# Kernel optimization log

Hardware: AMD Instinct MI355X
Metric: run time of the kernel (lower is better)

## Reference

```python
import jax, jax.numpy as jnp
import numpy as np

N_NODES = 50000
N_EDGES = 800000
LN_EPS = 1e-5


def _segment_softmax_aggr(msg, t, dst, n):
    # SoftmaxAggregation(learn=True): alpha = softmax(msg * t) per dest segment, out = sum(alpha * msg)
    logits = msg * t  # [E, C]
    m = jax.ops.segment_max(logits, dst, num_segments=n)
    m = jnp.where(jnp.isfinite(m), m, 0.0)  # empty segments -> 0 to keep exp finite
    e = jnp.exp(logits - m[dst])
    denom = jax.ops.segment_sum(e, dst, num_segments=n)
    alpha = e / jnp.maximum(denom[dst], 1e-16)
    return jax.ops.segment_sum(alpha * msg, dst, num_segments=n)


def _sage_conv(x, src, dst, wp, bp, t, wl, bl, wr):
    # project=True: messages come from relu(lin(x)); root term uses ORIGINAL x
    xp = jax.nn.relu(x @ wp + bp)
    msg = xp[src]                                   # [E, C] gather
    aggr = _segment_softmax_aggr(msg, t, dst, x.shape[0])
    out = aggr @ wl + bl + x @ wr
    # normalize=True: L2 normalize rows (eps as in F.normalize)
    nrm = jnp.maximum(jnp.linalg.norm(out, axis=-1, keepdims=True), 1e-12)
    return out / nrm


def _mem_pool(x, k, w_conv, wl, bl):
    # PyG MemPooling, tau=1: Student-t kernel 1/(1+d^2)
    H, K, F = k.shape
    kk = k.reshape(H * K, F)
    d2 = (jnp.sum(kk * kk, -1)[:, None] + jnp.sum(x * x, -1)[None, :]
          - 2.0 * kk @ x.T)                          # [H*K, N]
    d2 = jnp.maximum(d2, 0.0)
    dist = 1.0 / (1.0 + d2)
    dist = dist.reshape(H, K, -1).transpose(0, 2, 1)  # [H, N, K]
    S = dist / jnp.sum(dist, -1, keepdims=True)       # per-head normalize over clusters
    S = jnp.einsum('h,hnk->nk', w_conv, S)            # 1x1 conv mixing heads (no bias)
    S = jax.nn.softmax(S, axis=-1)                    # [N, K]
    xp = S.T @ x                                      # [K, F]
    return xp @ wl + bl                               # [K, out]


def setup_inputs() -> dict:
    key = jax.random.key(0)
    ks = jax.random.split(key, 20)
    rn = lambda i, shp, s: jax.random.normal(ks[i], shp, dtype=jnp.float32) * s
    inp = {
        'x': rn(0, (N_NODES, 64), 1.0),
        'edge_index': jax.random.randint(ks[1], (2, N_EDGES), 0, N_NODES, dtype=jnp.int32),
        'w_proj1': rn(2, (64, 64), 0.1), 'b_proj1': rn(3, (64,), 0.05),
        't1': jnp.ones((64,), jnp.float32),
        'w_l1': rn(4, (64, 256), 0.1), 'b_l1': rn(5, (256,), 0.05),
        'w_r1': rn(6, (64, 256), 0.1),
        'w_proj2': rn(7, (256, 256), 0.05), 'b_proj2': rn(8, (256,), 0.05),
        't2': jnp.ones((256,), jnp.float32),
        'w_l2': rn(9, (256, 128), 0.05), 'b_l2': rn(10, (128,), 0.05),
        'w_r2': rn(11, (256, 128), 0.05),
        'k_mem': rn(12, (4, 4, 128), 1.0),
        'w_conv': rn(13, (4,), 0.5),
        'w_memlin': rn(14, (128, 128), 0.08), 'b_memlin': rn(15, (128,), 0.05),
        'w_fx': rn(16, (128, 64), 0.08), 'b_fx': rn(17, (64,), 0.05),
        'gamma': jnp.ones((64,), jnp.float32),
        'beta': jnp.zeros((64,), jnp.float32),
    }
    return inp


def reference(x, edge_index, w_proj1, b_proj1, t1, w_l1, b_l1, w_r1,
              w_proj2, b_proj2, t2, w_l2, b_l2, w_r2,
              k_mem, w_conv, w_memlin, b_memlin, w_fx, b_fx, gamma, beta):
    src, dst = edge_index[0], edge_index[1]
    h = _sage_conv(x, src, dst, w_proj1, b_proj1, t1, w_l1, b_l1, w_r1)
    h = jax.nn.relu(h)                              # dropout = identity (eval)
    h = _sage_conv(h, src, dst, w_proj2, b_proj2, t2, w_l2, b_l2, w_r2)
    h = jax.nn.relu(h)
    pooled = _mem_pool(h, k_mem, w_conv, w_memlin, b_memlin)  # [4, 128]
    g = jnp.mean(pooled, axis=0, keepdims=True)     # global_mean_pool -> [1, 128]
    y = g @ w_fx + b_fx                             # [1, 64]
    mu = jnp.mean(y, -1, keepdims=True)
    var = jnp.var(y, -1, keepdims=True)
    y = (y - mu) / jnp.sqrt(var + LN_EPS) * gamma + beta
    return jax.nn.relu(y)
```

## Files before the change

### kernel.cpp

```cpp
#include <hip/hip_runtime.h>
#include <hip/hip_bf16.h>

#define N_NODES 50000
#define N_EDGES 800000
#define NB 196
#define PC_SLICES 2048
#define NWAVES 8192

typedef __attribute__((ext_vector_type(8))) short short8;
typedef __attribute__((ext_vector_type(4))) float f32x4;
typedef __attribute__((ext_vector_type(2))) float f32x2;

#define QSCALE2 (2.f / 255.f)
#define QINV2   127.5f
#define QSCALE1 (12.75f / 255.f)
#define QINV1   20.f

__device__ __forceinline__ float us2f(unsigned short u) {
    return __uint_as_float(((unsigned int)u) << 16);
}
__device__ __forceinline__ unsigned short f2bu(float f) {
    unsigned int u = __float_as_uint(f);
    unsigned int r = (u + 0x7fffu + ((u >> 16) & 1u)) >> 16;
    return (unsigned short)r;
}
__device__ __forceinline__ float exp2_hw(float x) {
    float r;
    __asm__("v_exp_f32 %0, %1" : "=v"(r) : "v"(x));
    return r;
}
__device__ __forceinline__ void async16(const void* g, void* l) {
    __builtin_amdgcn_global_load_lds(
        (const __attribute__((address_space(1))) unsigned int*)g,
        (__attribute__((address_space(3))) unsigned int*)l, 16, 0, 0);
}
#define LOG2E 1.44269504088896f

__global__ void k_hist(const int* __restrict__ dst, int* __restrict__ counts) {
    int e = blockIdx.x * 256 + threadIdx.x;
    if (e < N_EDGES) atomicAdd(&counts[dst[e]], 1);
}

__global__ __launch_bounds__(256) void k_scan1(const int* __restrict__ counts,
                                               int* __restrict__ row_ptr,
                                               int* __restrict__ partial) {
    __shared__ int sd[256];
    int t = threadIdx.x, i = blockIdx.x * 256 + t;
    int v = (i < N_NODES) ? counts[i] : 0;
    sd[t] = v;
    __syncthreads();
    for (int off = 1; off < 256; off <<= 1) {
        int o = (t >= off) ? sd[t - off] : 0;
        __syncthreads();
        sd[t] += o;
        __syncthreads();
    }
    if (i < N_NODES) row_ptr[i] = sd[t] - v;
    if (t == 255) partial[blockIdx.x] = sd[255];
}

__global__ __launch_bounds__(256) void k_scan3b(int* __restrict__ row_ptr,
                                                const int* __restrict__ partial,
                                                int* __restrict__ cursor) {
    __shared__ int sd[256];
    int t = threadIdx.x;
    sd[t] = (t < blockIdx.x) ? partial[t] : 0;
    __syncthreads();
    for (int off = 128; off > 0; off >>= 1) {
        if (t < off) sd[t] += sd[t + off];
        __syncthreads();
    }
    int base = sd[0];
    int i = blockIdx.x * 256 + t;
    if (i < N_NODES) {
        int v = row_ptr[i] + base;
        row_ptr[i] = v;
        cursor[i] = v;
    }
    if (blockIdx.x == 0 && t == 0) row_ptr[N_NODES] = N_EDGES;
}

__global__ void k_scatter(const int* __restrict__ src, const int* __restrict__ dst,
                          int* __restrict__ cursor, int* __restrict__ src_sorted) {
    int e = blockIdx.x * 256 + threadIdx.x;
    if (e < N_EDGES) {
        int d = dst[e];
        int pos = atomicAdd(&cursor[d], 1);
        src_sorted[pos] = src[e];
    }
}

__global__ __launch_bounds__(256) void k_split(const int* __restrict__ row_ptr,
                                               int* __restrict__ split) {
    int w = blockIdx.x * 256 + threadIdx.x;
    if (w > NWAVES) return;
    if (w == NWAVES) { split[w] = N_NODES; return; }
    int target = (int)((long long)w * N_EDGES / NWAVES);
    int lo = 0, hi = N_NODES;
    while (lo < hi) {
        int mid = (lo + hi) >> 1;
        if (row_ptr[mid] < target) lo = mid + 1; else hi = mid;
    }
    split[w] = lo;
}

#define XCAST_N (N_NODES * 64)
#define PREP_TOT (XCAST_N + 167936)
__global__ __launch_bounds__(256) void k_prep(const float* __restrict__ x,
                                              const float* __restrict__ wp1,
                                              const float* __restrict__ wl1,
                                              const float* __restrict__ wr1,
                                              const float* __restrict__ wp2,
                                              const float* __restrict__ wl2,
                                              const float* __restrict__ wr2,
                                              unsigned short* __restrict__ cat1,
                                              unsigned short* __restrict__ B0T,
                                              unsigned short* __restrict__ B1T,
                                              unsigned short* __restrict__ BP2T,
                                              unsigned short* __restrict__ B2T) {
    int idx = (blockIdx.x * 256 + threadIdx.x) * 4;
    if (idx < XCAST_N) {
        int i = idx >> 6, j = idx & 63;
        float4 v = *(const float4*)&x[idx];
        ushort4 o = { f2bu(v.x), f2bu(v.y), f2bu(v.z), f2bu(v.w) };
        *(ushort4*)&cat1[i * 128 + 64 + j] = o;
        return;
    }
    int w = idx - XCAST_N;
    if (w < 4096)  { float4 v = *(const float4*)&wp1[w]; int k = w >> 6, n = w & 63;
                     B0T[n*64+k]=f2bu(v.x); B0T[(n+1)*64+k]=f2bu(v.y);
                     B0T[(n+2)*64+k]=f2bu(v.z); B0T[(n+3)*64+k]=f2bu(v.w); return; }
    w -= 4096;
    if (w < 16384) { float4 v = *(const float4*)&wl1[w]; int k = w >> 8, n = w & 255;
                     B1T[n*128+k]=f2bu(v.x); B1T[(n+1)*128+k]=f2bu(v.y);
                     B1T[(n+2)*128+k]=f2bu(v.z); B1T[(n+3)*128+k]=f2bu(v.w); return; }
    w -= 16384;
    if (w < 16384) { float4 v = *(const float4*)&wr1[w]; int k = w >> 8, n = w & 255;
                     B1T[n*128+64+k]=f2bu(v.x); B1T[(n+1)*128+64+k]=f2bu(v.y);
                     B1T[(n+2)*128+64+k]=f2bu(v.z); B1T[(n+3)*128+64+k]=f2bu(v.w); return; }
    w -= 16384;
    if (w < 65536) { float4 v = *(const float4*)&wp2[w]; int k = w >> 8, n = w & 255;
                     BP2T[n*256+k]=f2bu(v.x); BP2T[(n+1)*256+k]=f2bu(v.y);
                     BP2T[(n+2)*256+k]=f2bu(v.z); BP2T[(n+3)*256+k]=f2bu(v.w); return; }
    w -= 65536;
    if (w < 32768) { float4 v = *(const float4*)&wl2[w]; int k = w >> 7, n = w & 127;
                     B2T[n*512+k]=f2bu(v.x); B2T[(n+1)*512+k]=f2bu(v.y);
                     B2T[(n+2)*512+k]=f2bu(v.z); B2T[(n+3)*512+k]=f2bu(v.w); return; }
    w -= 32768;
    if (w < 32768) { float4 v = *(const float4*)&wr2[w]; int k = w >> 7, n = w & 127;
                     B2T[n*512+256+k]=f2bu(v.x); B2T[(n+1)*512+256+k]=f2bu(v.y);
                     B2T[(n+2)*512+256+k]=f2bu(v.z); B2T[(n+3)*512+256+k]=f2bu(v.w); return; }
}

template<int K, int C, int LDA, int LDOUT, int OUT_OFF, int EP, int WPB, int MH>
__global__ __launch_bounds__(256, WPB) void k_gemm(const unsigned short* __restrict__ A,
                                                   const unsigned short* __restrict__ BT,
                                                   const float* __restrict__ bias,
                                                   void* __restrict__ outv,
                                                   const float* __restrict__ kmem,
                                                   const float* __restrict__ wconv,
                                                   float* __restrict__ Sm,
                                                   float qinv) {
    constexpr int NT = C / 16;
    constexpr int SAE = 64 * MH * 64;
    constexpr int SBE = C * 64;
    constexpr int STAGE_B = (SAE + SBE) * 2;
    constexpr int RPLD = (EP == 2) ? (C + 4) : ((EP == 3) ? (C + 16) : (C + 8));
    constexpr int RP_B = 64 * RPLD * (EP == 2 ? 4 : (EP == 3 ? 1 : 2));
    constexpr int SMEM_B = STAGE_B > RP_B ? STAGE_B : RP_B;
    constexpr int POOL_B = (EP == 2) ? (2048 * 4 + 64 + 16) : 16;
    __shared__ __align__(16) char smem[SMEM_B + POOL_B];
    unsigned short* sA = (unsigned short*)smem;
    unsigned short* sB = sA + SAE;
    float* kls  = (float*)(smem + SMEM_B);
    float* kk2s = kls + 2048;
    float* wcs  = kk2s + 16;

    int t = threadIdx.x;
    int wid = t >> 6, lane = t & 63;
    int lrow = lane & 15, quad = lane >> 4;
    int m0 = blockIdx.x * (64 * MH);

    if (EP == 2) {
        for (int i = t; i < 2048; i += 256) kls[i] = kmem[i];
        if (t < 4) wcs[t] = wconv[t];
        __syncthreads();
        if (t < 16) {
            float s = 0.f;
            for (int f = 0; f < 128; ++f) { float v = kls[t * 128 + f]; s += v * v; }
            kk2s[t] = s;
        }
    }

    f32x4 acc[MH][NT];
#pragma unroll
    for (int h = 0; h < MH; ++h)
#pragma unroll
        for (int nt = 0; nt < NT; ++nt)
#pragma unroll
            for (int r = 0; r < 4; ++r) acc[h][nt][r] = 0.f;

    for (int k0 = 0; k0 < K; k0 += 64) {
        __syncthreads();
        for (int i = t; i < 64 * MH * 8; i += 256) {
            int r = i >> 3, seg = i & 7;
            size_t m = (size_t)(m0 + r);
            async16(&A[m * LDA + k0 + ((seg ^ (r & 7)) << 3)],
                    (char*)sA + (size_t)(i - lane) * 16);
        }
        for (int i = t; i < C * 8; i += 256) {
            int n = i >> 3, seg = i & 7;
            async16(&BT[(size_t)n * K + k0 + ((seg ^ (n & 7)) << 3)],
                    (char*)sB + (size_t)(i - lane) * 16);
        }
        __syncthreads();
#pragma unroll
        for (int kk = 0; kk < 2; ++kk) {
            int sw = lrow & 7;
            short8 av[MH];
#pragma unroll
            for (int h = 0; h < MH; ++h)
                av[h] = *(const short8*)&sA[(h * 64 + wid * 16 + lrow) * 64 +
                                            (((kk * 4 + quad) ^ sw) << 3)];
#pragma unroll
            for (int nt = 0; nt < NT; ++nt) {
                short8 bfg = *(const short8*)&sB[(nt * 16 + lrow) * 64 +
                                                 (((kk * 4 + quad) ^ sw) << 3)];
#pragma unroll
                for (int h = 0; h < MH; ++h)
                    acc[h][nt] = __builtin_amdgcn_mfma_f32_16x16x32_bf16(av[h], bfg, acc[h][nt], 0, 0, 0);
            }
        }
    }

#pragma unroll
    for (int h = 0; h < MH; ++h) {
#pragma unroll
        for (int nt = 0; nt < NT; ++nt) {
            float bv = bias[nt * 16 + lrow];
#pragma unroll
            for (int r = 0; r < 4; ++r) acc[h][nt][r] += bv;
        }
        if (EP == 1 || EP == 2) {
#pragma unroll
            for (int r = 0; r < 4; ++r) {
                float ss = 0.f;
#pragma unroll
                for (int nt = 0; nt < NT; ++nt) ss += acc[h][nt][r] * acc[h][nt][r];
                ss += __shfl_xor(ss, 1);
                ss += __shfl_xor(ss, 2);
                ss += __shfl_xor(ss, 4);
                ss += __shfl_xor(ss, 8);
                float rinv = 1.f / fmaxf(sqrtf(ss), 1e-12f);
#pragma unroll
                for (int nt = 0; nt < NT; ++nt)
                    acc[h][nt][r] = fmaxf(acc[h][nt][r] * rinv, 0.f);
            }
        } else {
#pragma unroll
            for (int nt = 0; nt < NT; ++nt)
#pragma unroll
                for (int r = 0; r < 4; ++r) acc[h][nt][r] = fmaxf(acc[h][nt][r], 0.f);
        }
    }

    __syncthreads();
#pragma unroll
    for (int h = 0; h < MH; ++h) {
        if (EP == 2) {
            float* rp = (float*)smem;
#pragma unroll
            for (int nt = 0; nt < NT; ++nt)
#pragma unroll
                for (int r = 0; r < 4; ++r)
                    rp[(wid * 16 + quad * 4 + r) * RPLD + nt * 16 + lrow] = acc[h][nt][r];
            __syncthreads();
            float* outp = (float*)outv;
            for (int i = t; i < 64 * C / 4; i += 256) {
                int f = i * 4, r = f / C, c = f % C;
                int m = m0 + h * 64 + r;
                if (m < N_NODES)
                    *(float4*)&outp[(size_t)m * LDOUT + OUT_OFF + c] = *(const float4*)&rp[r * RPLD + c];
            }
            {
                int row = t >> 2, p = t & 3;
                int cbase = p * 32;
                float dots[16];
#pragma unroll
                for (int k = 0; k < 16; ++k) dots[k] = 0.f;
                float x2 = 0.f;
#pragma unroll
                for (int j = 0; j < 8; ++j) {
                    int c4 = (j + p * 2) & 7;
                    float4 xv = *(const float4*)&rp[row * RPLD + cbase + c4 * 4];
                    x2 += xv.x * xv.x + xv.y * xv.y + xv.z * xv.z + xv.w * xv.w;
#pragma unroll
                    for (int k = 0; k < 16; ++k) {
                        float4 kv = *(const float4*)&kls[k * 128 + cbase + c4 * 4];
                        dots[k] += xv.x * kv.x + xv.y * kv.y + xv.z * kv.z + xv.w * kv.w;
                    }
                }
#pragma unroll
                for (int k = 0; k < 16; ++k) {
                    dots[k] += __shfl_xor(dots[k], 1);
                    dots[k] += __shfl_xor(dots[k], 2);
                }
                x2 += __shfl_xor(x2, 1);
                x2 += __shfl_xor(x2, 2);
                if (p == 0) {
                    int m = m0 + h * 64 + row;
                    if (m < N_NODES) {
                        float dist[16];
#pragma unroll
                        for (int k = 0; k < 16; ++k) {
                            float d2 = fmaxf(kk2s[k] + x2 - 2.f * dots[k], 0.f);
                            dist[k] = 1.f / (1.f + d2);
                        }
                        float s0 = 0.f, s1 = 0.f, s2 = 0.f, s3 = 0.f;
#pragma unroll
                        for (int hh = 0; hh < 4; ++hh) {
                            float den = dist[hh * 4] + dist[hh * 4 + 1] +
                                        dist[hh * 4 + 2] + dist[hh * 4 + 3];
                            float inv = wcs[hh] / den;
                            s0 += dist[hh * 4 + 0] * inv;
                            s1 += dist[hh * 4 + 1] * inv;
                            s2 += dist[hh * 4 + 2] * inv;
                            s3 += dist[hh * 4 + 3] * inv;
                        }
                        float mx = fmaxf(fmaxf(s0, s1), fmaxf(s2, s3));
                        float e0 = __expf(s0 - mx), e1 = __expf(s1 - mx);
                        float e2 = __expf(s2 - mx), e3 = __expf(s3 - mx);
                        float inv = 1.f / (e0 + e1 + e2 + e3);
                        *(float4*)&Sm[(size_t)m * 4] =
                            make_float4(e0 * inv, e1 * inv, e2 * inv, e3 * inv);
                    }
                }
            }
            __syncthreads();
        } else if (EP == 3) {
            unsigned char* rp = (unsigned char*)smem;
#pragma unroll
            for (int nt = 0; nt < NT; ++nt)
#pragma unroll
                for (int r = 0; r < 4; ++r) {
                    float q = fminf(__builtin_rintf(acc[h][nt][r] * qinv), 255.f);
                    rp[(wid * 16 + quad * 4 + r) * RPLD + nt * 16 + lrow] = (unsigned char)(int)q;
                }
            __syncthreads();
            unsigned char* outp = (unsigned char*)outv;
            for (int i = t; i < 64 * C / 16; i += 256) {
                int f = i * 16, r = f / C, c = f % C;
                int m = m0 + h * 64 + r;
                if (m < N_NODES)
                    *(uint4*)&outp[(size_t)m * LDOUT + OUT_OFF + c] = *(const uint4*)&rp[r * RPLD + c];
            }
            __syncthreads();
        } else {
            unsigned short* rp = (unsigned short*)smem;
#pragma unroll
            for (int nt = 0; nt < NT; ++nt)
#pragma unroll
                for (int r = 0; r < 4; ++r)
                    rp[(wid * 16 + quad * 4 + r) * RPLD + nt * 16 + lrow] = f2bu(acc[h][nt][r]);
            __syncthreads();
            unsigned short* outp = (unsigned short*)outv;
            for (int i = t; i < 64 * C / 8; i += 256) {
                int f = i * 8, r = f / C, c = f % C;
                int m = m0 + h * 64 + r;
                if (m < N_NODES)
                    *(uint4*)&outp[(size_t)m * LDOUT + OUT_OFF + c] = *(const uint4*)&rp[r * RPLD + c];
            }
            __syncthreads();
        }
    }
}

__global__ __launch_bounds__(256, 4) void k_aggr256(const unsigned char* __restrict__ xp,
                                                    const float* __restrict__ tvec,
                                                    const int* __restrict__ row_ptr,
                                                    const int* __restrict__ srcs,
                                                    const int* __restrict__ split,
                                                    unsigned short* __restrict__ outp) {
    int t = threadIdx.x & 63;
    int w = blockIdx.x * 4 + (threadIdx.x >> 6);
    float4 tv4 = *(const float4*)&tvec[t * 4];
    f32x2 tv01 = {tv4.x * (LOG2E * QSCALE2), tv4.y * (LOG2E * QSCALE2)};
    f32x2 tv23 = {tv4.z * (LOG2E * QSCALE2), tv4.w * (LOG2E * QSCALE2)};
    int n    = __builtin_amdgcn_readfirstlane(split[w]);
    int nend = __builtin_amdgcn_readfirstlane(split[w + 1]);
    if (n >= nend) return;
    int e    = __builtin_amdgcn_readfirstlane(row_ptr[n]);
    int eend = __builtin_amdgcn_readfirstlane(row_ptr[nend]);
    int rp_next = __builtin_amdgcn_readfirstlane(row_ptr[n + 1]);
    f32x2 se01 = {0.f, 0.f}, se23 = {0.f, 0.f};
    f32x2 sem01 = {0.f, 0.f}, sem23 = {0.f, 0.f};

#define FINALIZE()                                                             \
    {                                                                          \
        ushort4 o;                                                             \
        o.x = f2bu(QSCALE2 * sem01.x / fmaxf(se01.x, 1e-16f));                 \
        o.y = f2bu(QSCALE2 * sem01.y / fmaxf(se01.y, 1e-16f));                 \
        o.z = f2bu(QSCALE2 * sem23.x / fmaxf(se23.x, 1e-16f));                 \
        o.w = f2bu(QSCALE2 * sem23.y / fmaxf(se23.y, 1e-16f));                 \
        *(ushort4*)&outp[(size_t)n * 512 + t * 4] = o;                         \
        se01 = (f32x2){0.f, 0.f}; se23 = (f32x2){0.f, 0.f};                    \
        sem01 = (f32x2){0.f, 0.f}; sem23 = (f32x2){0.f, 0.f};                  \
        ++n;                                                                   \
        rp_next = (n < nend) ? __builtin_amdgcn_readfirstlane(row_ptr[n + 1])  \
                             : 0x7FFFFFFF;                                     \
    }
#define EDGE_BODY(VV)                                                          \
    {                                                                          \
        f32x2 m01 = {(float)((VV) & 0xFFu), (float)(((VV) >> 8) & 0xFFu)};     \
        f32x2 m23 = {(float)(((VV) >> 16) & 0xFFu), (float)((VV) >> 24)};      \
        f32x2 l01 = m01 * tv01, l23 = m23 * tv23;                              \
        f32x2 w01, w23;                                                        \
        w01.x = exp2_hw(l01.x); w01.y = exp2_hw(l01.y);                        \
        w23.x = exp2_hw(l23.x); w23.y = exp2_hw(l23.y);                        \
        se01 += w01; se23 += w23;                                              \
        sem01 = __builtin_elementwise_fma(w01, m01, sem01);                    \
        sem23 = __builtin_elementwise_fma(w23, m23, sem23);                    \
    }

    while (rp_next <= e) FINALIZE();

    while (e < eend) {
        unsigned int v[16];
        int rem = eend - e;
        int cnt = rem > 16 ? 16 : rem;
        if (cnt == 16) {
#pragma unroll
            for (int j = 0; j < 16; ++j) {
                const unsigned char* p = xp + (size_t)srcs[e + j] * 256;
                v[j] = *(const unsigned int*)&p[t * 4];
            }
        } else {
#pragma unroll
            for (int j = 0; j < 16; ++j) {
                int ee = e + j;
                ee = ee < eend ? ee : eend - 1;
                const unsigned char* p = xp + (size_t)srcs[ee] * 256;
                v[j] = *(const unsigned int*)&p[t * 4];
            }
        }
#pragma unroll
        for (int j = 0; j < 16; ++j) {
            if (j < cnt) {
                EDGE_BODY(v[j])
                while (e + j + 1 == rp_next) FINALIZE();
            }
        }
        e += cnt;
    }
#undef EDGE_BODY
#undef FINALIZE
}

__global__ __launch_bounds__(256, 4) void k_aggr64(const unsigned char* __restrict__ xp,
                                                   const float* __restrict__ tvec,
                                                   const int* __restrict__ row_ptr,
                                                   const int* __restrict__ srcs,
                                                   const int* __restrict__ split,
                                                   unsigned short* __restrict__ outp) {
    int c = threadIdx.x & 63;
    int w = blockIdx.x * 4 + (threadIdx.x >> 6);
    float tv = tvec[c] * (LOG2E * QSCALE1);
    int n    = __builtin_amdgcn_readfirstlane(split[w]);
    int nend = __builtin_amdgcn_readfirstlane(split[w + 1]);
    if (n >= nend) return;
    int e    = __builtin_amdgcn_readfirstlane(row_ptr[n]);
    int eend = __builtin_amdgcn_readfirstlane(row_ptr[nend]);
    int rp_next = __builtin_amdgcn_readfirstlane(row_ptr[n + 1]);
    float se = 0.f, sem = 0.f;

#define FIN1()                                                                 \
    {                                                                          \
        outp[(size_t)n * 128 + c] = f2bu(QSCALE1 * sem / fmaxf(se, 1e-16f));   \
        se = 0.f; sem = 0.f;                                                   \
        ++n;                                                                   \
        rp_next = (n < nend) ? __builtin_amdgcn_readfirstlane(row_ptr[n + 1])  \
                             : 0x7FFFFFFF;                                     \
    }

    while (rp_next <= e) FIN1();

    while (e < eend) {
        unsigned char v[16];
        int rem = eend - e;
        int cnt = rem > 16 ? 16 : rem;
        if (cnt == 16) {
#pragma unroll
            for (int j = 0; j < 16; ++j)
                v[j] = xp[(size_t)srcs[e + j] * 64 + c];
        } else {
#pragma unroll
            for (int j = 0; j < 16; ++j) {
                int ee = e + j;
                ee = ee < eend ? ee : eend - 1;
                v[j] = xp[(size_t)srcs[ee] * 64 + c];
            }
        }
#pragma unroll
        for (int j = 0; j < 16; ++j) {
            if (j < cnt) {
                float msg = (float)v[j];
                float wv = exp2_hw(msg * tv);
                se += wv;
                sem = fmaf(wv, msg, sem);
                while (e + j + 1 == rp_next) FIN1();
            }
        }
        e += cnt;
    }
#undef FIN1
}

__global__ __launch_bounds__(256) void k_pool_c(const float* __restrict__ h2,
                                                const float* __restrict__ Sm,
                                                float* __restrict__ part) {
    int t = threadIdx.x;
    int c = t & 127, sub = t >> 7;
    int slice = blockIdx.x * 2 + sub;
    float a0 = 0.f, a1 = 0.f, a2 = 0.f, a3 = 0.f;
    for (int n = slice; n < N_NODES; n += PC_SLICES) {
        float xv = h2[(size_t)n * 128 + c];
        float4 sv = *(const float4*)&Sm[(size_t)n * 4];
        a0 = fmaf(sv.x, xv, a0);
        a1 = fmaf(sv.y, xv, a1);
        a2 = fmaf(sv.z, xv, a2);
        a3 = fmaf(sv.w, xv, a3);
    }
    float* p = &part[(size_t)slice * 512];
    p[0 * 128 + c] = a0;
    p[1 * 128 + c] = a1;
    p[2 * 128 + c] = a2;
    p[3 * 128 + c] = a3;
}

__global__ __launch_bounds__(256) void k_pool_b(const float* __restrict__ part,
                                                float* __restrict__ pooled) {
    int j = blockIdx.x;
    float s = 0.f;
    for (int b = threadIdx.x; b < PC_SLICES; b += 256) s += part[(size_t)b * 512 + j];
#pragma unroll
    for (int off = 32; off > 0; off >>= 1) s += __shfl_xor(s, off);
    __shared__ float red[4];
    int lane = threadIdx.x & 63, wid = threadIdx.x >> 6;
    if (lane == 0) red[wid] = s;
    __syncthreads();
    if (threadIdx.x == 0) pooled[j] = red[0] + red[1] + red[2] + red[3];
}

__global__ __launch_bounds__(128) void k_final(const float* __restrict__ pooled,
                                               const float* __restrict__ wmem,
                                               const float* __restrict__ bmem,
                                               const float* __restrict__ wfx,
                                               const float* __restrict__ bfx,
                                               const float* __restrict__ gamma,
                                               const float* __restrict__ beta,
                                               float* __restrict__ out) {
    __shared__ float gx[128], g[128];
    int t = threadIdx.x;
    gx[t] = 0.25f * (pooled[t] + pooled[128 + t] + pooled[256 + t] + pooled[384 + t]);
    __syncthreads();
    float acc = bmem[t];
    for (int f = 0; f < 128; ++f) acc = fmaf(gx[f], wmem[f * 128 + t], acc);
    g[t] = acc;
    __syncthreads();
    if (t < 64) {
        float y = bfx[t];
        for (int f = 0; f < 128; ++f) y = fmaf(g[f], wfx[f * 64 + t], y);
        float s = y, s2 = y * y;
#pragma unroll
        for (int off = 32; off > 0; off >>= 1) {
            s += __shfl_xor(s, off);
            s2 += __shfl_xor(s2, off);
        }
        float mu = s * (1.f / 64.f);
        float var = s2 * (1.f / 64.f) - mu * mu;
        float v = (y - mu) / sqrtf(var + 1e-5f) * gamma[t] + beta[t];
        out[t] = fmaxf(v, 0.f);
    }
}

extern "C" void kernel_launch(void* const* d_in, const int* in_sizes, int n_in,
                              void* d_out, int out_size, void* d_ws, size_t ws_size,
                              hipStream_t stream) {
    const float* x        = (const float*)d_in[0];
    const int*   ei       = (const int*)  d_in[1];
    const float* w_proj1  = (const float*)d_in[2];
    const float* b_proj1  = (const float*)d_in[3];
    const float* t1       = (const float*)d_in[4];
    const float* w_l1     = (const float*)d_in[5];
    const float* b_l1     = (const float*)d_in[6];
    const float* w_r1     = (const float*)d_in[7];
    const float* w_proj2  = (const float*)d_in[8];
    const float* b_proj2  = (const float*)d_in[9];
    const float* t2       = (const float*)d_in[10];
    const float* w_l2     = (const float*)d_in[11];
    const float* b_l2     = (const float*)d_in[12];
    const float* w_r2     = (const float*)d_in[13];
    const float* k_mem    = (const float*)d_in[14];
    const float* w_conv   = (const float*)d_in[15];
    const float* w_memlin = (const float*)d_in[16];
    const float* b_memlin = (const float*)d_in[17];
    const float* w_fx     = (const float*)d_in[18];
    const float* b_fx     = (const float*)d_in[19];
    const float* gamma    = (const float*)d_in[20];
    const float* beta     = (const float*)d_in[21];
    const int* src = ei;
    const int* dst = ei + N_EDGES;
    (void)in_sizes; (void)n_in; (void)out_size; (void)ws_size;

    char* W = (char*)d_ws;
    const size_t MB = 1024 * 1024;
    int*   row_ptr    = (int*)(W + 0);
    int*   cursor     = (int*)(W + 256 * 1024);
    int*   partial    = (int*)(W + 512 * 1024);
    int*   split      = (int*)(W + 520 * 1024);
    int*   src_sorted = (int*)(W + 768 * 1024);
    unsigned short* cat1 = (unsigned short*)(W + 4 * MB);
    unsigned char*  xp1  = (unsigned char*)(W + 17 * MB);
    unsigned short* cat2 = (unsigned short*)(W + 24 * MB);
    unsigned char*  xp2  = (unsigned char*)(W + 76 * MB);
    float* h2     = (float*)(W + 102 * MB);
    float* Sm     = (float*)(W + 128 * MB);
    float* pooled = (float*)(W + 131 * MB);
    unsigned short* B0T  = (unsigned short*)(W + 133 * MB);
    unsigned short* B1T  = (unsigned short*)(W + 134 * MB);
    unsigned short* BP2T = (unsigned short*)(W + 135 * MB);
    unsigned short* B2T  = (unsigned short*)(W + 136 * MB);
    float* part   = (float*)(W + 140 * MB);

    hipMemsetAsync(cursor, 0, N_NODES * sizeof(int), stream);
    k_hist<<<(N_EDGES + 255) / 256, 256, 0, stream>>>(dst, cursor);
    k_scan1<<<NB, 256, 0, stream>>>(cursor, row_ptr, partial);
    k_scan3b<<<NB, 256, 0, stream>>>(row_ptr, partial, cursor);
    k_split<<<(NWAVES + 1 + 255) / 256, 256, 0, stream>>>(row_ptr, split);
    k_scatter<<<(N_EDGES + 255) / 256, 256, 0, stream>>>(src, dst, cursor, src_sorted);

    k_prep<<<(PREP_TOT / 4 + 255) / 256, 256, 0, stream>>>(
        x, w_proj1, w_l1, w_r1, w_proj2, w_l2, w_r2, cat1, B0T, B1T, BP2T, B2T);

    const int GB = (N_NODES + 127) / 128;
    const int AGB = NWAVES / 4;

    k_gemm<64, 64, 128, 64, 0, 3, 4, 2><<<GB, 256, 0, stream>>>(
        cat1 + 64, B0T, b_proj1, xp1, nullptr, nullptr, nullptr, QINV1);
    k_aggr64<<<AGB, 256, 0, stream>>>(xp1, t1, row_ptr, src_sorted, split, cat1);
    k_gemm<128, 256, 128, 512, 256, 1, 3, 2><<<GB, 256, 0, stream>>>(
        cat1, B1T, b_l1, cat2, nullptr, nullptr, nullptr, 0.f);

    k_gemm<256, 256, 512, 256, 0, 3, 3, 2><<<GB, 256, 0, stream>>>(
        cat2 + 256, BP2T, b_proj2, xp2, nullptr, nullptr, nullptr, QINV2);
    k_aggr256<<<AGB, 256, 0, stream>>>(xp2, t2, row_ptr, src_sorted, split, cat2);
    k_gemm<512, 128, 512, 128, 0, 2, 3, 2><<<GB, 256, 0, stream>>>(
        cat2, B2T, b_l2, h2, k_mem, w_conv, Sm, 0.f);

    k_pool_c<<<PC_SLICES / 2, 256, 0, stream>>>(h2, Sm, part);
    k_pool_b<<<512, 256, 0, stream>>>(part, pooled);
    k_final<<<1, 128, 0, stream>>>(pooled, w_memlin, b_memlin, w_fx, b_fx, gamma, beta,
                                   (float*)d_out);
}
```

Baseline: 376.7 us.

## Replace global per-node atomic scatter with two-level bucketed CSR build

The CSR construction now works in two passes. Edges are first bucketed by destination block of 256 nodes using 196 global atomic counters, with src and the local dst offset packed into one int. A per-block kernel then scatters inside each bucket using shared-memory atomics. The aim is to replace scattered global atomics and random writes with more local access, at the cost of an extra pass, an extra launch and a temporary buffer. Packing src into 16 bits assumes node ids stay below 65536.

```diff
diff --git a/kernel.cpp b/kernel.cpp
--- a/kernel.cpp
+++ b/kernel.cpp
@@ -60,8 +60,7 @@
 }
 
 __global__ __launch_bounds__(256) void k_scan3b(int* __restrict__ row_ptr,
-                                                const int* __restrict__ partial,
-                                                int* __restrict__ cursor) {
+                                                const int* __restrict__ partial) {
     __shared__ int sd[256];
     int t = threadIdx.x;
     sd[t] = (t < blockIdx.x) ? partial[t] : 0;
@@ -72,21 +71,39 @@
     }
     int base = sd[0];
     int i = blockIdx.x * 256 + t;
-    if (i < N_NODES) {
-        int v = row_ptr[i] + base;
-        row_ptr[i] = v;
-        cursor[i] = v;
-    }
+    if (i < N_NODES) row_ptr[i] += base;
     if (blockIdx.x == 0 && t == 0) row_ptr[N_NODES] = N_EDGES;
 }
 
-__global__ void k_scatter(const int* __restrict__ src, const int* __restrict__ dst,
-                          int* __restrict__ cursor, int* __restrict__ src_sorted) {
+__global__ void k_binit(const int* __restrict__ row_ptr, int* __restrict__ bcur) {
+    int b = threadIdx.x;
+    if (b < NB) bcur[b] = row_ptr[b * 256];
+}
+
+__global__ void k_bucket(const int* __restrict__ src, const int* __restrict__ dst,
+                         int* __restrict__ bcur, int* __restrict__ tmp) {
     int e = blockIdx.x * 256 + threadIdx.x;
     if (e < N_EDGES) {
         int d = dst[e];
-        int pos = atomicAdd(&cursor[d], 1);
-        src_sorted[pos] = src[e];
+        int pos = atomicAdd(&bcur[d >> 8], 1);
+        tmp[pos] = src[e] | ((d & 255) << 16);
+    }
+}
+
+__global__ __launch_bounds__(256) void k_scatter2(const int* __restrict__ row_ptr,
+                                                  const int* __restrict__ tmp,
+                                                  int* __restrict__ src_sorted) {
+    __shared__ int lcur[256];
+    int b = blockIdx.x, t = threadIdx.x;
+    int n0 = b * 256;
+    int nhi = n0 + 256 < N_NODES ? n0 + 256 : N_NODES;
+    if (n0 + t < nhi) lcur[t] = row_ptr[n0 + t];
+    __syncthreads();
+    int ebeg = row_ptr[n0], eend = row_ptr[nhi];
+    for (int i = ebeg + t; i < eend; i += 256) {
+        int w = tmp[i];
+        int pos = atomicAdd(&lcur[(w >> 16) & 255], 1);
+        src_sorted[pos] = w & 0xFFFF;
     }
 }
 
@@ -615,8 +632,9 @@
     char* W = (char*)d_ws;
     const size_t MB = 1024 * 1024;
     int*   row_ptr    = (int*)(W + 0);
-    int*   cursor     = (int*)(W + 256 * 1024);
+    int*   counts     = (int*)(W + 256 * 1024);
     int*   partial    = (int*)(W + 512 * 1024);
+    int*   bcur       = (int*)(W + 512 * 1024 + 4096);
     int*   split      = (int*)(W + 520 * 1024);
     int*   src_sorted = (int*)(W + 768 * 1024);
     unsigned short* cat1 = (unsigned short*)(W + 4 * MB);
@@ -631,13 +649,16 @@
     unsigned short* BP2T = (unsigned short*)(W + 135 * MB);
     unsigned short* B2T  = (unsigned short*)(W + 136 * MB);
     float* part   = (float*)(W + 140 * MB);
-
-    hipMemsetAsync(cursor, 0, N_NODES * sizeof(int), stream);
-    k_hist<<<(N_EDGES + 255) / 256, 256, 0, stream>>>(dst, cursor);
-    k_scan1<<<NB, 256, 0, stream>>>(cursor, row_ptr, partial);
-    k_scan3b<<<NB, 256, 0, stream>>>(row_ptr, partial, cursor);
+    int*   tmp_e  = (int*)(W + 144 * MB);
+
+    hipMemsetAsync(counts, 0, N_NODES * sizeof(int), stream);
+    k_hist<<<(N_EDGES + 255) / 256, 256, 0, stream>>>(dst, counts);
+    k_scan1<<<NB, 256, 0, stream>>>(counts, row_ptr, partial);
+    k_scan3b<<<NB, 256, 0, stream>>>(row_ptr, partial);
+    k_binit<<<1, 256, 0, stream>>>(row_ptr, bcur);
     k_split<<<(NWAVES + 1 + 255) / 256, 256, 0, stream>>>(row_ptr, split);
-    k_scatter<<<(N_EDGES + 255) / 256, 256, 0, stream>>>(src, dst, cursor, src_sorted);
+    k_bucket<<<(N_EDGES + 255) / 256, 256, 0, stream>>>(src, dst, bcur, tmp_e);
+    k_scatter2<<<NB, 256, 0, stream>>>(row_ptr, tmp_e, src_sorted);
 
     k_prep<<<(PREP_TOT / 4 + 255) / 256, 256, 0, stream>>>(
         x, w_proj1, w_l1, w_r1, w_proj2, w_l2, w_r2, cat1, B0T, B1T, BP2T, B2T);
```

New measurement: 792.3 us. 110% more time.
